# Kernel tuning notes

Hardware: AMD Instinct MI355X
Metric: run time of the kernel (lower is better)

## Reference

```python
import jax, jax.numpy as jnp
import numpy as np


def setup_inputs() -> dict:
    key = jax.random.key(0)
    k1, k2, k3, kw, kb = jax.random.split(key, 5)
    B, IN, OUT = 32, 64, 256
    bound = 1.0 / np.sqrt(IN)
    return {
        "input1": jax.random.normal(k1, (B, IN), dtype=jnp.float32),
        "input2": jax.random.normal(k2, (B, IN), dtype=jnp.float32),
        "input3": jax.random.normal(k3, (B, IN), dtype=jnp.float32),
        "weight": jax.random.uniform(kw, (OUT, IN, IN, IN), dtype=jnp.float32, minval=-bound, maxval=bound),
        "b": jax.random.uniform(kb, (OUT,), dtype=jnp.float32, minval=-bound, maxval=bound),
    }


def reference(input1, input2, input3, weight, b):
    # Four-way trilinear contraction: out[b,a] = sum_{n,m,o} x1[b,n] x2[b,m] x3[b,o] W[a,n,m,o]
    # Form the small rank-1 outer product per batch [B, n, m, o] (B*64^3 elems),
    # then a single GEMM against the flattened weight -- avoids any [B, out, in, in]
    # pairwise intermediate.
    x123 = jnp.einsum('bn,bm,bo->bnmo', input1, input2, input3)
    out = jnp.einsum('bnmo,anmo->ba', x123, weight)
    return out + b
```

## Files before the change

### kernel.cpp

```cpp
#include <hip/hip_runtime.h>
#include <hip/hip_bf16.h>

typedef __bf16 bf16x8 __attribute__((ext_vector_type(8)));
typedef float  f32x4  __attribute__((ext_vector_type(4)));

#define K_TOTAL (64*64*64)
#define B_DIM   32
#define A_DIM   256
#define G_SPLIT 256
#define K_CHUNK (K_TOTAL / G_SPLIT)

__global__ __launch_bounds__(256) void build_x123(
    const float* __restrict__ x1, const float* __restrict__ x2,
    const float* __restrict__ x3, __bf16* __restrict__ X)
{
    int t  = blockIdx.x * blockDim.x + threadIdx.x;
    int o8 = t & 7;
    int m  = (t >> 3) & 63;
    int n  = (t >> 9) & 63;
    int b  = t >> 15;

    float p12 = x1[b * 64 + n] * x2[b * 64 + m];
    const f32x4* x3v = reinterpret_cast<const f32x4*>(x3 + b * 64 + o8 * 8);
    f32x4 c0 = x3v[0];
    f32x4 c1 = x3v[1];

    bf16x8 outv;
#pragma unroll
    for (int i = 0; i < 4; ++i) {
        outv[i]     = (__bf16)(p12 * c0[i]);
        outv[i + 4] = (__bf16)(p12 * c1[i]);
    }
    *reinterpret_cast<bf16x8*>(X + (size_t)t * 8) = outv;
}

__global__ __launch_bounds__(1024, 4) void gemm_splitk(
    const __bf16* __restrict__ X,
    const float*  __restrict__ W,
    float* __restrict__ partials)
{
    const int g     = blockIdx.x;
    const int kbase = g * K_CHUNK;
    const int wave  = threadIdx.x >> 6;
    const int lane  = threadIdx.x & 63;
    const int l15   = lane & 15;
    const int lg    = lane >> 4;
    const int a0    = wave * 16;

    f32x4 acc0 = {0.f, 0.f, 0.f, 0.f};
    f32x4 acc1 = {0.f, 0.f, 0.f, 0.f};

    const __bf16* Arow0 = X + (size_t)l15        * K_TOTAL + kbase + lg * 8;
    const __bf16* Arow1 = X + (size_t)(l15 + 16) * K_TOTAL + kbase + lg * 8;
    const float*  Brow  = W + (size_t)(a0 + l15) * K_TOTAL + kbase + lg * 8;

#pragma unroll 4
    for (int ks = 0; ks < K_CHUNK; ks += 32) {
        bf16x8 afrag0 = *reinterpret_cast<const bf16x8*>(Arow0 + ks);
        bf16x8 afrag1 = *reinterpret_cast<const bf16x8*>(Arow1 + ks);
        f32x4 w0 = *reinterpret_cast<const f32x4*>(Brow + ks);
        f32x4 w1 = *reinterpret_cast<const f32x4*>(Brow + ks + 4);

        bf16x8 bfrag;
#pragma unroll
        for (int i = 0; i < 4; ++i) {
            bfrag[i]     = (__bf16)w0[i];
            bfrag[i + 4] = (__bf16)w1[i];
        }
        acc0 = __builtin_amdgcn_mfma_f32_16x16x32_bf16(afrag0, bfrag, acc0, 0, 0, 0);
        acc1 = __builtin_amdgcn_mfma_f32_16x16x32_bf16(afrag1, bfrag, acc1, 0, 0, 0);
    }

    float* p = partials + (size_t)g * (B_DIM * A_DIM);
#pragma unroll
    for (int r = 0; r < 4; ++r) {
        p[(lg * 4 + r) * A_DIM      + a0 + l15] = acc0[r];
        p[(16 + lg * 4 + r) * A_DIM + a0 + l15] = acc1[r];
    }
}

__global__ __launch_bounds__(256) void reduce_partials(
    const float* __restrict__ partials, const float* __restrict__ bias,
    float* __restrict__ out)
{
    int blk = blockIdx.x;
    int b   = blk >> 3;
    int ac  = blk & 7;
    int t   = threadIdx.x;
    int a   = ac * 32 + (t & 31);
    int gs  = t >> 5;

    float s = 0.f;
#pragma unroll 4
    for (int i = 0; i < 32; ++i) {
        int g = gs * 32 + i;
        s += partials[((size_t)g * B_DIM + b) * A_DIM + a];
    }

    __shared__ float red[256];
    red[t] = s;
    __syncthreads();
    if (t < 32) {
        float tot = red[t];
#pragma unroll
        for (int j = 1; j < 8; ++j) tot += red[t + 32 * j];
        out[b * A_DIM + a] = tot + bias[a];
    }
}

extern "C" void kernel_launch(void* const* d_in, const int* in_sizes, int n_in,
                              void* d_out, int out_size, void* d_ws, size_t ws_size,
                              hipStream_t stream) {
    const float* x1   = (const float*)d_in[0];
    const float* x2   = (const float*)d_in[1];
    const float* x3   = (const float*)d_in[2];
    const float* W    = (const float*)d_in[3];
    const float* bias = (const float*)d_in[4];
    float* out = (float*)d_out;

    __bf16* X       = (__bf16*)d_ws;
    float* partials = (float*)((char*)d_ws + (size_t)B_DIM * K_TOTAL * 2);

    hipLaunchKernelGGL(build_x123, dim3((B_DIM * K_TOTAL / 8) / 256), dim3(256),
                       0, stream, x1, x2, x3, X);
    hipLaunchKernelGGL(gemm_splitk, dim3(G_SPLIT), dim3(1024),
                       0, stream, X, W, partials);
    hipLaunchKernelGGL(reduce_partials, dim3(256), dim3(256),
                       0, stream, partials, bias, out);
}
```

Measured before the change: 393.5 us.

## Stage bf16 weight tiles in LDS and block X layout for coalesced GEMM

Restructures the split-K GEMM into 2048 smaller blocks, each converting a 64x512 slice of fp32 weights to bf16 in shared memory with fully contiguous row loads. The activation product is written in a k-blocked layout so MFMA operand loads are contiguous. This aims to raise memory-level parallelism and coalescing on the dominant weight stream. In exchange, X is read four times and the partials buffer doubles in size, making the reduction heavier.

```diff
diff --git a/kernel.cpp b/kernel.cpp
--- a/kernel.cpp
+++ b/kernel.cpp
@@ -2,80 +2,99 @@
 #include <hip/hip_bf16.h>
 
 typedef __bf16 bf16x8 __attribute__((ext_vector_type(8)));
+typedef __bf16 bf16x4 __attribute__((ext_vector_type(4)));
 typedef float  f32x4  __attribute__((ext_vector_type(4)));
 
 #define K_TOTAL (64*64*64)
 #define B_DIM   32
 #define A_DIM   256
-#define G_SPLIT 256
-#define K_CHUNK (K_TOTAL / G_SPLIT)
+#define KC      512
+#define NKC     (K_TOTAL/KC)
+#define ATILE   64
+#define NAT     (A_DIM/ATILE)
+#define WSTRIDE 520
 
-__global__ __launch_bounds__(256) void build_x123(
+__global__ __launch_bounds__(256) void build_xp(
     const float* __restrict__ x1, const float* __restrict__ x2,
-    const float* __restrict__ x3, __bf16* __restrict__ X)
+    const float* __restrict__ x3, __bf16* __restrict__ Xp)
 {
     int t  = blockIdx.x * blockDim.x + threadIdx.x;
-    int o8 = t & 7;
-    int m  = (t >> 3) & 63;
-    int n  = (t >> 9) & 63;
+    int k8 = t & 32767;
     int b  = t >> 15;
+    int o8 = k8 & 7;
+    int m  = (k8 >> 3) & 63;
+    int n  = k8 >> 9;
 
     float p12 = x1[b * 64 + n] * x2[b * 64 + m];
-    const f32x4* x3v = reinterpret_cast<const f32x4*>(x3 + b * 64 + o8 * 8);
-    f32x4 c0 = x3v[0];
-    f32x4 c1 = x3v[1];
+    f32x4 c0 = *reinterpret_cast<const f32x4*>(x3 + b * 64 + o8 * 8);
+    f32x4 c1 = *reinterpret_cast<const f32x4*>(x3 + b * 64 + o8 * 8 + 4);
 
-    bf16x8 outv;
+    bf16x8 v;
 #pragma unroll
     for (int i = 0; i < 4; ++i) {
-        outv[i]     = (__bf16)(p12 * c0[i]);
-        outv[i + 4] = (__bf16)(p12 * c1[i]);
+        v[i]     = (__bf16)(p12 * c0[i]);
+        v[i + 4] = (__bf16)(p12 * c1[i]);
     }
-    *reinterpret_cast<bf16x8*>(X + (size_t)t * 8) = outv;
+    int k = k8 * 8;
+    size_t off = (size_t)(k >> 5) * 1024 + b * 32 + (k & 31);
+    *reinterpret_cast<bf16x8*>(Xp + off) = v;
 }
 
-__global__ __launch_bounds__(1024, 4) void gemm_splitk(
-    const __bf16* __restrict__ X,
+__global__ __launch_bounds__(256, 2) void gemm_staged(
+    const __bf16* __restrict__ Xp,
     const float*  __restrict__ W,
     float* __restrict__ partials)
 {
-    const int g     = blockIdx.x;
-    const int kbase = g * K_CHUNK;
-    const int wave  = threadIdx.x >> 6;
-    const int lane  = threadIdx.x & 63;
-    const int l15   = lane & 15;
-    const int lg    = lane >> 4;
-    const int a0    = wave * 16;
+    __shared__ __bf16 w_lds[ATILE * WSTRIDE];
+
+    const int bid  = blockIdx.x;
+    const int at   = bid & (NAT - 1);
+    const int kc   = bid >> 2;
+    const int wv   = threadIdx.x >> 6;
+    const int lane = threadIdx.x & 63;
+
+    const float* wbase = W + (size_t)(at * ATILE + wv * 16) * K_TOTAL + kc * KC;
+#pragma unroll 4
+    for (int i = 0; i < 16; ++i) {
+        const float* wr = wbase + (size_t)i * K_TOTAL;
+        f32x4 lo = *reinterpret_cast<const f32x4*>(wr + lane * 4);
+        f32x4 hi = *reinterpret_cast<const f32x4*>(wr + 256 + lane * 4);
+        bf16x4 blo, bhi;
+#pragma unroll
+        for (int j = 0; j < 4; ++j) {
+            blo[j] = (__bf16)lo[j];
+            bhi[j] = (__bf16)hi[j];
+        }
+        __bf16* dst = w_lds + (wv * 16 + i) * WSTRIDE;
+        *reinterpret_cast<bf16x4*>(dst + lane * 4)       = blo;
+        *reinterpret_cast<bf16x4*>(dst + 256 + lane * 4) = bhi;
+    }
+    __syncthreads();
+
+    const int l15 = lane & 15;
+    const int lg  = lane >> 4;
 
     f32x4 acc0 = {0.f, 0.f, 0.f, 0.f};
     f32x4 acc1 = {0.f, 0.f, 0.f, 0.f};
 
-    const __bf16* Arow0 = X + (size_t)l15        * K_TOTAL + kbase + lg * 8;
-    const __bf16* Arow1 = X + (size_t)(l15 + 16) * K_TOTAL + kbase + lg * 8;
-    const float*  Brow  = W + (size_t)(a0 + l15) * K_TOTAL + kbase + lg * 8;
+    const __bf16* arow = Xp + (size_t)(kc * (KC / 32)) * 1024 + l15 * 32 + lg * 8;
+    const __bf16* brow = w_lds + (wv * 16 + l15) * WSTRIDE + lg * 8;
 
 #pragma unroll 4
-    for (int ks = 0; ks < K_CHUNK; ks += 32) {
-        bf16x8 afrag0 = *reinterpret_cast<const bf16x8*>(Arow0 + ks);
-        bf16x8 afrag1 = *reinterpret_cast<const bf16x8*>(Arow1 + ks);
-        f32x4 w0 = *reinterpret_cast<const f32x4*>(Brow + ks);
-        f32x4 w1 = *reinterpret_cast<const f32x4*>(Brow + ks + 4);
-
-        bf16x8 bfrag;
-#pragma unroll
-        for (int i = 0; i < 4; ++i) {
-            bfrag[i]     = (__bf16)w0[i];
-            bfrag[i + 4] = (__bf16)w1[i];
-        }
-        acc0 = __builtin_amdgcn_mfma_f32_16x16x32_bf16(afrag0, bfrag, acc0, 0, 0, 0);
-        acc1 = __builtin_amdgcn_mfma_f32_16x16x32_bf16(afrag1, bfrag, acc1, 0, 0, 0);
+    for (int kk = 0; kk < KC / 32; ++kk) {
+        bf16x8 a0 = *reinterpret_cast<const bf16x8*>(arow + kk * 1024);
+        bf16x8 a1 = *reinterpret_cast<const bf16x8*>(arow + kk * 1024 + 512);
+        bf16x8 bb = *reinterpret_cast<const bf16x8*>(brow + kk * 32);
+        acc0 = __builtin_amdgcn_mfma_f32_16x16x32_bf16(a0, bb, acc0, 0, 0, 0);
+        acc1 = __builtin_amdgcn_mfma_f32_16x16x32_bf16(a1, bb, acc1, 0, 0, 0);
     }
 
-    float* p = partials + (size_t)g * (B_DIM * A_DIM);
+    float* p = partials + (size_t)kc * (B_DIM * A_DIM)
+                        + (at * ATILE + wv * 16 + l15);
 #pragma unroll
     for (int r = 0; r < 4; ++r) {
-        p[(lg * 4 + r) * A_DIM      + a0 + l15] = acc0[r];
-        p[(16 + lg * 4 + r) * A_DIM + a0 + l15] = acc1[r];
+        p[(lg * 4 + r) * A_DIM]        = acc0[r];
+        p[(16 + lg * 4 + r) * A_DIM]   = acc1[r];
     }
 }
 
@@ -92,9 +111,9 @@
 
     float s = 0.f;
 #pragma unroll 4
-    for (int i = 0; i < 32; ++i) {
-        int g = gs * 32 + i;
-        s += partials[((size_t)g * B_DIM + b) * A_DIM + a];
+    for (int i = 0; i < NKC / 8; ++i) {
+        int kc = gs * (NKC / 8) + i;
+        s += partials[((size_t)kc * B_DIM + b) * A_DIM + a];
     }
 
     __shared__ float red[256];
@@ -118,13 +137,13 @@
     const float* bias = (const float*)d_in[4];
     float* out = (float*)d_out;
 
-    __bf16* X       = (__bf16*)d_ws;
+    __bf16* Xp      = (__bf16*)d_ws;
     float* partials = (float*)((char*)d_ws + (size_t)B_DIM * K_TOTAL * 2);
 
-    hipLaunchKernelGGL(build_x123, dim3((B_DIM * K_TOTAL / 8) / 256), dim3(256),
-                       0, stream, x1, x2, x3, X);
-    hipLaunchKernelGGL(gemm_splitk, dim3(G_SPLIT), dim3(1024),
-                       0, stream, X, W, partials);
+    hipLaunchKernelGGL(build_xp, dim3((B_DIM * K_TOTAL / 8) / 256), dim3(256),
+                       0, stream, x1, x2, x3, Xp);
+    hipLaunchKernelGGL(gemm_staged, dim3(NAT * NKC), dim3(256),
+                       0, stream, Xp, W, partials);
     hipLaunchKernelGGL(reduce_partials, dim3(256), dim3(256),
                        0, stream, partials, bias, out);
 }
```

Measured after the change: 393.3 us. Within noise of the previous version (-0.0%).
